# Kernel tuning notes

Measured on AMD Instinct MI355X. Metric: run time of the kernel, lower is better.

The kernel has to match this reference:

```python
import jax, jax.numpy as jnp
import numpy as np

E, H, F, K = 8, 1024, 4096, 2  # experts, hidden, intermediate, top-k
B, S = 4, 2048


def setup_inputs() -> dict:
    key = jax.random.key(0)
    ks = jax.random.split(key, 6)
    x = jax.random.normal(ks[0], (B, S, H), dtype=jnp.float32)
    gate_w = jax.random.normal(ks[1], (H, E), dtype=jnp.float32) * 0.02
    gate_b = jnp.zeros((E,), dtype=jnp.float32)
    Wg = jax.random.normal(ks[2], (E, H, F), dtype=jnp.float32) * 0.02
    Wu = jax.random.normal(ks[3], (E, H, F), dtype=jnp.float32) * 0.02
    Wd = jax.random.normal(ks[4], (E, F, H), dtype=jnp.float32) * 0.02
    return {"x": x, "gate_w": gate_w, "gate_b": gate_b, "Wg": Wg, "Wu": Wu, "Wd": Wd}


def _moe_forward(x, gate_w, gate_b, Wg, Wu, Wd):
    xf = x.reshape(-1, x.shape[-1])                      # [T, H]
    T = xf.shape[0]
    logits = xf @ gate_w + gate_b                        # [T, E]  (gate_logit)
    top_vals, top_idx = jax.lax.top_k(logits, K)         # [T, K]
    # scatter top-k logits into -inf background, softmax -> zero weight for unselected experts
    sparse = jnp.full_like(logits, -jnp.inf)
    sparse = sparse.at[jnp.arange(T)[:, None], top_idx].set(top_vals)
    gate_weights = jax.nn.softmax(sparse, axis=-1)       # [T, E], exactly 0 off top-k

    # sum_e w_e * Expert_e(x); scan over the small expert axis to bound memory
    def expert_step(acc, params):
        wg, wu, wd, w = params                           # wg:[H,F] wu:[H,F] wd:[F,H] w:[T]
        h = jax.nn.silu(xf @ wg) * (xf @ wu)             # [T, F]
        y = h @ wd                                       # [T, H]
        return acc + w[:, None] * y, None

    acc0 = jnp.zeros_like(xf)
    acc, _ = jax.lax.scan(expert_step, acc0, (Wg, Wu, Wd, gate_weights.T))
    return acc.reshape(x.shape), logits


def reference(x, gate_w, gate_b, Wg, Wu, Wd):
    return _moe_forward(x, gate_w, gate_b, Wg, Wu, Wd)
```

## Files before the change

### kernel.cpp

```cpp
#include <hip/hip_runtime.h>
#include <cstdint>

#define TTOK 8192
#define HID  1024
#define FFD  4096
#define NEXP 8
#define NASSIGN 16384

typedef __attribute__((ext_vector_type(8))) short bf16x8;
typedef __attribute__((ext_vector_type(4))) float f32x4;

__device__ __forceinline__ unsigned short f2bf(float f) {
  unsigned int u = __builtin_bit_cast(unsigned int, f);
  u += 0x7FFFu + ((u >> 16) & 1u);
  return (unsigned short)(u >> 16);
}

__device__ __forceinline__ void gload16(const unsigned short* g, unsigned short* l) {
  __builtin_amdgcn_global_load_lds(
      (const __attribute__((address_space(1))) unsigned int*)g,
      (__attribute__((address_space(3))) unsigned int*)l, 16, 0, 0);
}

__device__ __forceinline__ int swz_col(int t) {
  return (((t & 3) ^ ((t >> 3) & 3)) << 3);
}


__global__ void zero_counts_kernel(int* counts) {
  if (threadIdx.x < NEXP) counts[threadIdx.x] = 0;
}

__global__ void gate_kernel(const float* __restrict__ x,
                            const float* __restrict__ gw,
                            const float* __restrict__ gb,
                            float* __restrict__ logits_out,
                            int* __restrict__ counts,
                            int* __restrict__ te, int* __restrict__ tp,
                            float* __restrict__ tw) {
  const int lane = threadIdx.x & 63;
  const int wib  = threadIdx.x >> 6;
  const int t = blockIdx.x * 4 + wib;
  const float* xr = x + (size_t)t * HID;

  float acc[NEXP];
#pragma unroll
  for (int e = 0; e < NEXP; ++e) acc[e] = 0.f;

#pragma unroll
  for (int i = 0; i < HID / 64; ++i) {
    int h = lane + 64 * i;
    float xv = xr[h];
    const float* g = gw + h * NEXP;
#pragma unroll
    for (int e = 0; e < NEXP; ++e) acc[e] += xv * g[e];
  }
#pragma unroll
  for (int off = 32; off; off >>= 1)
#pragma unroll
    for (int e = 0; e < NEXP; ++e) acc[e] += __shfl_xor(acc[e], off);
#pragma unroll
  for (int e = 0; e < NEXP; ++e) acc[e] += gb[e];

  if (lane < NEXP) logits_out[(size_t)t * NEXP + lane] = acc[lane];

  if (lane == 0) {
    int e0 = 0; float v0 = acc[0];
#pragma unroll
    for (int e = 1; e < NEXP; ++e) if (acc[e] > v0) { v0 = acc[e]; e0 = e; }
    int e1 = -1; float v1 = -3.4e38f;
#pragma unroll
    for (int e = 0; e < NEXP; ++e) if (e != e0 && acc[e] > v1) { v1 = acc[e]; e1 = e; }
    float s = __expf(v1 - v0);
    float w0 = 1.f / (1.f + s);
    float w1 = s * w0;
    int p0 = atomicAdd(&counts[e0], 1);
    int p1 = atomicAdd(&counts[e1], 1);
    te[t * 2] = e0; te[t * 2 + 1] = e1;
    tp[t * 2] = p0; tp[t * 2 + 1] = p1;
    tw[t * 2] = w0; tw[t * 2 + 1] = w1;
  }
}

__global__ void scatter_kernel(const int* __restrict__ counts, int* __restrict__ offsets,
                               const int* __restrict__ te, const int* __restrict__ tp,
                               const float* __restrict__ tw,
                               int* __restrict__ tok_of, float* __restrict__ wt_of,
                               int* __restrict__ asn_of) {
  __shared__ int offs[NEXP];
  if (threadIdx.x == 0) {
    int run = 0;
    for (int e = 0; e < NEXP; ++e) { offs[e] = run; offsets[e] = run; run += counts[e]; }
  }
  __syncthreads();
  for (int t = threadIdx.x; t < TTOK; t += blockDim.x) {
#pragma unroll
    for (int j = 0; j < 2; ++j) {
      int e = te[t * 2 + j];
      int a = offs[e] + tp[t * 2 + j];
      tok_of[a] = t;
      wt_of[a] = tw[t * 2 + j];
      asn_of[t * 2 + j] = a;
    }
  }
}


__global__ void convert_x_kernel(const float* __restrict__ x, unsigned short* __restrict__ xb) {
  size_t i = ((size_t)blockIdx.x * 256 + threadIdx.x) * 8;
  float4 a = *(const float4*)(x + i);
  float4 b = *(const float4*)(x + i + 4);
  union { unsigned short us[8]; uint4 v; } u;
  u.us[0] = f2bf(a.x); u.us[1] = f2bf(a.y); u.us[2] = f2bf(a.z); u.us[3] = f2bf(a.w);
  u.us[4] = f2bf(b.x); u.us[5] = f2bf(b.y); u.us[6] = f2bf(b.z); u.us[7] = f2bf(b.w);
  *(uint4*)(xb + i) = u.v;
}

__global__ void transpose_cvt_kernel(const float* __restrict__ src,
                                     unsigned short* __restrict__ dst, int R, int C) {
  __shared__ float tile[32][33];
  const int r0 = blockIdx.y * 32, c0 = blockIdx.x * 32;
  const size_t base = (size_t)blockIdx.z * R * C;
  src += base; dst += base;
#pragma unroll
  for (int i = threadIdx.y; i < 32; i += 8)
    tile[i][threadIdx.x] = src[(size_t)(r0 + i) * C + c0 + threadIdx.x];
  __syncthreads();
#pragma unroll
  for (int i = threadIdx.y; i < 32; i += 8)
    dst[(size_t)(c0 + i) * R + r0 + threadIdx.x] = f2bf(tile[threadIdx.x][i]);
}


#define UBM 256
#define UBN 128
#define BK  32

__global__ __launch_bounds__(512, 2) void moe_up_kernel(
    const unsigned short* __restrict__ xb,
    const unsigned short* __restrict__ WgT,
    const unsigned short* __restrict__ WuT,
    const int* __restrict__ counts, const int* __restrict__ offsets,
    const int* __restrict__ tok_of,
    unsigned short* __restrict__ hbuf)
{
  const int e = blockIdx.x & 7;
  const int mblk = blockIdx.x >> 3;
  const int cnt = counts[e];
  if (mblk * UBM >= cnt) return;
  const int off = offsets[e];
  const int n0 = blockIdx.y * UBN;

  __shared__ __align__(16) unsigned short As[4 * UBM * BK];
  __shared__ __align__(16) unsigned short Bgs[4 * UBN * BK];
  __shared__ __align__(16) unsigned short Bus[4 * UBN * BK];
  __shared__ int toks[UBM];

  const int tid = threadIdx.x;
  const int lane = tid & 63;
  const int w = tid >> 6;

  for (int i = tid; i < UBM; i += 512) {
    int a = off + mblk * UBM + i;
    if (a > NASSIGN - 1) a = NASSIGN - 1;
    toks[i] = tok_of[a];
  }
  __syncthreads();

  const int trow = tid >> 2;
  const int tcol = swz_col(tid);
  const unsigned short* a_src0 = xb + (size_t)toks[trow] * HID + tcol;
  const unsigned short* a_src1 = xb + (size_t)toks[128 + trow] * HID + tcol;
  const unsigned short* bg_src = WgT + ((size_t)e * FFD + n0 + trow) * HID + tcol;
  const unsigned short* bu_src = WuT + ((size_t)e * FFD + n0 + trow) * HID + tcol;

  auto STAGE_A = [&](int kt) {
    const int b = kt & 3, k0 = kt * BK;
    gload16(a_src0 + k0, As + b * (UBM * BK) + tid * 8);
    gload16(a_src1 + k0, As + b * (UBM * BK) + 4096 + tid * 8);
  };
  auto STAGE_B = [&](int kt) {
    const int b = kt & 3, k0 = kt * BK;
    gload16(bg_src + k0, Bgs + b * (UBN * BK) + tid * 8);
    gload16(bu_src + k0, Bus + b * (UBN * BK) + tid * 8);
  };

  const int lr = lane & 15, s = lane >> 4;
  const int rdswz = ((s ^ ((lr >> 1) & 3)) << 3);
  const int wm = w >> 1, wn = w & 1;
  const int arow = wm * 64 + lr;
  const int brow = wn * 64 + lr;

  f32x4 accg[4][4] = {};
  f32x4 accu[4][4] = {};

  STAGE_A(0); STAGE_B(0);
  STAGE_A(1); STAGE_B(1);
  STAGE_A(2); STAGE_B(2);

  const int NT = HID / BK;
#pragma unroll 4
  for (int kt = 0; kt < NT; ++kt) {
    const int b = kt & 3;
    asm volatile("s_waitcnt vmcnt(8)" ::: "memory");
    __builtin_amdgcn_s_barrier();

    const unsigned short* ab = As  + b * (UBM * BK);
    const unsigned short* gb = Bgs + b * (UBN * BK);
    const unsigned short* ub = Bus + b * (UBN * BK);

    bf16x8 af[4], bgf[4];
#pragma unroll
    for (int m = 0; m < 4; ++m)
      af[m] = *(const bf16x8*)(ab + (arow + m * 16) * BK + rdswz);
#pragma unroll
    for (int n = 0; n < 4; ++n)
      bgf[n] = *(const bf16x8*)(gb + (brow + n * 16) * BK + rdswz);
    if (kt + 3 < NT) STAGE_A(kt + 3);
    __builtin_amdgcn_s_barrier();

    __builtin_amdgcn_s_setprio(1);
#pragma unroll
    for (int m = 0; m < 4; ++m)
#pragma unroll
      for (int n = 0; n < 4; ++n)
        accg[m][n] = __builtin_amdgcn_mfma_f32_16x16x32_bf16(af[m], bgf[n], accg[m][n], 0, 0, 0);
    __builtin_amdgcn_s_setprio(0);

    bf16x8 buf_[4];
#pragma unroll
    for (int n = 0; n < 4; ++n)
      buf_[n] = *(const bf16x8*)(ub + (brow + n * 16) * BK + rdswz);
    if (kt + 3 < NT) STAGE_B(kt + 3);
    __builtin_amdgcn_s_barrier();

    __builtin_amdgcn_s_setprio(1);
#pragma unroll
    for (int m = 0; m < 4; ++m)
#pragma unroll
      for (int n = 0; n < 4; ++n)
        accu[m][n] = __builtin_amdgcn_mfma_f32_16x16x32_bf16(af[m], buf_[n], accu[m][n], 0, 0, 0);
    __builtin_amdgcn_s_setprio(0);
  }

  const int crb = (lane >> 4) * 4, cc = lane & 15;
#pragma unroll
  for (int m = 0; m < 4; ++m)
#pragma unroll
    for (int n = 0; n < 4; ++n)
#pragma unroll
      for (int r = 0; r < 4; ++r) {
        int lrow = wm * 64 + m * 16 + crb + r;
        int grow = mblk * UBM + lrow;
        if (grow < cnt) {
          size_t a = (size_t)off + grow;
          float g = accg[m][n][r];
          float u = accu[m][n][r];
          float sg = g / (1.0f + __expf(-g));
          hbuf[a * FFD + (n0 + wn * 64 + n * 16 + cc)] = f2bf(sg * u);
        }
      }
}

#define DBM 128
#define DBN 256

__global__ __launch_bounds__(512, 2) void moe_down_kernel(
    const unsigned short* __restrict__ hb,
    const unsigned short* __restrict__ WdT,
    const int* __restrict__ counts, const int* __restrict__ offsets,
    float* __restrict__ ypart)
{
  const int e = blockIdx.x & 7;
  const int mblk = blockIdx.x >> 3;
  const int cnt = counts[e];
  if (mblk * DBM >= cnt) return;
  const int off = offsets[e];
  const int n0 = blockIdx.y * DBN;

  __shared__ __align__(16) unsigned short As[4 * DBM * BK];
  __shared__ __align__(16) unsigned short Bs[4 * DBN * BK];

  const int tid = threadIdx.x;
  const int lane = tid & 63;
  const int w = tid >> 6;

  const int trow = tid >> 2;
  const int tcol = swz_col(tid);
  int arow_g = off + mblk * DBM + trow;
  if (arow_g > NASSIGN - 1) arow_g = NASSIGN - 1;
  const unsigned short* a_src  = hb + (size_t)arow_g * FFD + tcol;
  const unsigned short* b_src0 = WdT + ((size_t)e * HID + n0 + trow) * FFD + tcol;
  const unsigned short* b_src1 = WdT + ((size_t)e * HID + n0 + 128 + trow) * FFD + tcol;

  auto STAGE = [&](int kt) {
    const int b = kt & 3, k0 = kt * BK;
    gload16(a_src  + k0, As + b * (DBM * BK) + tid * 8);
    gload16(b_src0 + k0, Bs + b * (DBN * BK) + tid * 8);
    gload16(b_src1 + k0, Bs + b * (DBN * BK) + 4096 + tid * 8);
  };

  const int lr = lane & 15, s = lane >> 4;
  const int rdswz = ((s ^ ((lr >> 1) & 3)) << 3);
  const int wm = w >> 2, wn = w & 3;
  const int arow = wm * 64 + lr;
  const int brow = wn * 64 + lr;

  f32x4 acc[4][4] = {};

  STAGE(0); STAGE(1); STAGE(2);

  const int NT = FFD / BK;
#pragma unroll 4
  for (int kt = 0; kt < NT; ++kt) {
    const int b = kt & 3;
    asm volatile("s_waitcnt vmcnt(6)" ::: "memory");
    __builtin_amdgcn_s_barrier();

    const unsigned short* ab = As + b * (DBM * BK);
    const unsigned short* bb = Bs + b * (DBN * BK);

    bf16x8 af[4], bf_[4];
#pragma unroll
    for (int m = 0; m < 4; ++m)
      af[m] = *(const bf16x8*)(ab + (arow + m * 16) * BK + rdswz);
#pragma unroll
    for (int n = 0; n < 4; ++n)
      bf_[n] = *(const bf16x8*)(bb + (brow + n * 16) * BK + rdswz);
    if (kt + 3 < NT) STAGE(kt + 3);
    __builtin_amdgcn_s_barrier();

    __builtin_amdgcn_s_setprio(1);
#pragma unroll
    for (int m = 0; m < 4; ++m)
#pragma unroll
      for (int n = 0; n < 4; ++n)
        acc[m][n] = __builtin_amdgcn_mfma_f32_16x16x32_bf16(af[m], bf_[n], acc[m][n], 0, 0, 0);
    __builtin_amdgcn_s_setprio(0);
  }

  const int crb = (lane >> 4) * 4, cc = lane & 15;
#pragma unroll
  for (int m = 0; m < 4; ++m)
#pragma unroll
    for (int n = 0; n < 4; ++n)
#pragma unroll
      for (int r = 0; r < 4; ++r) {
        int lrow = wm * 64 + m * 16 + crb + r;
        int grow = mblk * DBM + lrow;
        if (grow < cnt)
          ypart[((size_t)off + grow) * HID + (n0 + wn * 64 + n * 16 + cc)] = acc[m][n][r];
      }
}

__global__ void combine_kernel(const float* __restrict__ ypart,
                               const int* __restrict__ asn_of,
                               const float* __restrict__ wt_of,
                               float* __restrict__ y) {
  const int t = blockIdx.x;
  const int a0 = asn_of[t * 2], a1 = asn_of[t * 2 + 1];
  const float w0 = wt_of[a0], w1 = wt_of[a1];
  const int c = threadIdx.x * 4;
  float4 p0 = *(const float4*)&ypart[(size_t)a0 * HID + c];
  float4 p1 = *(const float4*)&ypart[(size_t)a1 * HID + c];
  float4 r;
  r.x = w0 * p0.x + w1 * p1.x;
  r.y = w0 * p0.y + w1 * p1.y;
  r.z = w0 * p0.z + w1 * p1.z;
  r.w = w0 * p0.w + w1 * p1.w;
  *(float4*)&y[(size_t)t * HID + c] = r;
}


extern "C" void kernel_launch(void* const* d_in, const int* in_sizes, int n_in,
                              void* d_out, int out_size, void* d_ws, size_t ws_size,
                              hipStream_t stream) {
  const float* x  = (const float*)d_in[0];
  const float* gw = (const float*)d_in[1];
  const float* gb = (const float*)d_in[2];
  const float* Wg = (const float*)d_in[3];
  const float* Wu = (const float*)d_in[4];
  const float* Wd = (const float*)d_in[5];
  float* out = (float*)d_out;
  float* logits = out + (size_t)TTOK * HID;

  char* ws = (char*)d_ws;
  size_t o = 0;
  auto carve = [&](size_t b) { char* p = ws + o; o += (b + 255) & ~(size_t)255; return p; };
  int*   counts  = (int*)carve(NEXP * 4);
  int*   offsets = (int*)carve(NEXP * 4);
  int*   te      = (int*)carve((size_t)TTOK * 2 * 4);
  int*   tp      = (int*)carve((size_t)TTOK * 2 * 4);
  float* tw      = (float*)carve((size_t)TTOK * 2 * 4);
  int*   tok_of  = (int*)carve((size_t)NASSIGN * 4);
  float* wt_of   = (float*)carve((size_t)NASSIGN * 4);
  int*   asn_of  = (int*)carve((size_t)TTOK * 2 * 4);
  unsigned short* xb  = (unsigned short*)carve((size_t)TTOK * HID * 2);
  unsigned short* WgT = (unsigned short*)carve((size_t)NEXP * FFD * HID * 2);
  unsigned short* WuT = (unsigned short*)carve((size_t)NEXP * FFD * HID * 2);
  unsigned short* WdT = (unsigned short*)carve((size_t)NEXP * HID * FFD * 2);
  unsigned short* hb  = (unsigned short*)carve((size_t)NASSIGN * FFD * 2);
  float* ypart        = (float*)carve((size_t)NASSIGN * HID * 4);
  (void)ws_size; (void)in_sizes; (void)n_in; (void)out_size;

  zero_counts_kernel<<<dim3(1), dim3(64), 0, stream>>>(counts);
  gate_kernel<<<dim3(TTOK / 4), dim3(256), 0, stream>>>(x, gw, gb, logits, counts, te, tp, tw);
  scatter_kernel<<<dim3(1), dim3(256), 0, stream>>>(counts, offsets, te, tp, tw, tok_of, wt_of, asn_of);
  convert_x_kernel<<<dim3((TTOK * HID) / 2048), dim3(256), 0, stream>>>(x, xb);
  transpose_cvt_kernel<<<dim3(FFD / 32, HID / 32, NEXP), dim3(32, 8), 0, stream>>>(Wg, WgT, HID, FFD);
  transpose_cvt_kernel<<<dim3(FFD / 32, HID / 32, NEXP), dim3(32, 8), 0, stream>>>(Wu, WuT, HID, FFD);
  transpose_cvt_kernel<<<dim3(HID / 32, FFD / 32, NEXP), dim3(32, 8), 0, stream>>>(Wd, WdT, FFD, HID);
  moe_up_kernel<<<dim3(NEXP * 32, FFD / UBN), dim3(512), 0, stream>>>(xb, WgT, WuT, counts, offsets, tok_of, hb);
  moe_down_kernel<<<dim3(NEXP * 64, HID / DBN), dim3(512), 0, stream>>>(hb, WdT, counts, offsets, ypart);
  combine_kernel<<<dim3(TTOK), dim3(256), 0, stream>>>(ypart, asn_of, wt_of, out);
}
```

Measured before the change: 1.084 ms.

## Rework MoE GEMM pipelines to BK=64 double-buffered tiles with larger down-proj tile

```diff
diff --git a/kernel.cpp b/kernel.cpp
--- a/kernel.cpp
+++ b/kernel.cpp
@@ -20,10 +20,6 @@
   __builtin_amdgcn_global_load_lds(
       (const __attribute__((address_space(1))) unsigned int*)g,
       (__attribute__((address_space(3))) unsigned int*)l, 16, 0, 0);
-}
-
-__device__ __forceinline__ int swz_col(int t) {
-  return (((t & 3) ^ ((t >> 3) & 3)) << 3);
 }
 
 
@@ -132,11 +128,12 @@
 }
 
 
+#define BK 64
+
 #define UBM 256
 #define UBN 128
-#define BK  32
-
-__global__ __launch_bounds__(512, 2) void moe_up_kernel(
+
+__global__ __launch_bounds__(512, 1) void moe_up_kernel(
     const unsigned short* __restrict__ xb,
     const unsigned short* __restrict__ WgT,
     const unsigned short* __restrict__ WuT,
@@ -151,9 +148,9 @@
   const int off = offsets[e];
   const int n0 = blockIdx.y * UBN;
 
-  __shared__ __align__(16) unsigned short As[4 * UBM * BK];
-  __shared__ __align__(16) unsigned short Bgs[4 * UBN * BK];
-  __shared__ __align__(16) unsigned short Bus[4 * UBN * BK];
+  __shared__ __align__(16) unsigned short As[2][UBM * BK];
+  __shared__ __align__(16) unsigned short Bgs[2][UBN * BK];
+  __shared__ __align__(16) unsigned short Bus[2][UBN * BK];
   __shared__ int toks[UBM];
 
   const int tid = threadIdx.x;
@@ -167,105 +164,124 @@
   }
   __syncthreads();
 
-  const int trow = tid >> 2;
-  const int tcol = swz_col(tid);
-  const unsigned short* a_src0 = xb + (size_t)toks[trow] * HID + tcol;
-  const unsigned short* a_src1 = xb + (size_t)toks[128 + trow] * HID + tcol;
-  const unsigned short* bg_src = WgT + ((size_t)e * FFD + n0 + trow) * HID + tcol;
-  const unsigned short* bu_src = WuT + ((size_t)e * FFD + n0 + trow) * HID + tcol;
-
-  auto STAGE_A = [&](int kt) {
-    const int b = kt & 3, k0 = kt * BK;
-    gload16(a_src0 + k0, As + b * (UBM * BK) + tid * 8);
-    gload16(a_src1 + k0, As + b * (UBM * BK) + 4096 + tid * 8);
+  const int st = tid & 7, sr = tid >> 3;
+  const int scol = ((st ^ (sr & 7)) << 3);
+  const unsigned short* a_src[4];
+#pragma unroll
+  for (int i = 0; i < 4; ++i)
+    a_src[i] = xb + (size_t)toks[i * 64 + sr] * HID + scol;
+  const unsigned short* bg_src[2];
+  const unsigned short* bu_src[2];
+#pragma unroll
+  for (int i = 0; i < 2; ++i) {
+    bg_src[i] = WgT + ((size_t)e * FFD + n0 + i * 64 + sr) * HID + scol;
+    bu_src[i] = WuT + ((size_t)e * FFD + n0 + i * 64 + sr) * HID + scol;
+  }
+
+  auto STAGE = [&](int kt) {
+    const int b = kt & 1, k0 = kt * BK;
+#pragma unroll
+    for (int i = 0; i < 4; ++i) gload16(a_src[i] + k0, &As[b][i * 4096 + tid * 8]);
+#pragma unroll
+    for (int i = 0; i < 2; ++i) {
+      gload16(bg_src[i] + k0, &Bgs[b][i * 4096 + tid * 8]);
+      gload16(bu_src[i] + k0, &Bus[b][i * 4096 + tid * 8]);
+    }
   };
-  auto STAGE_B = [&](int kt) {
-    const int b = kt & 3, k0 = kt * BK;
-    gload16(bg_src + k0, Bgs + b * (UBN * BK) + tid * 8);
-    gload16(bu_src + k0, Bus + b * (UBN * BK) + tid * 8);
-  };
-
-  const int lr = lane & 15, s = lane >> 4;
-  const int rdswz = ((s ^ ((lr >> 1) & 3)) << 3);
-  const int wm = w >> 1, wn = w & 1;
-  const int arow = wm * 64 + lr;
-  const int brow = wn * 64 + lr;
-
-  f32x4 accg[4][4] = {};
-  f32x4 accu[4][4] = {};
-
-  STAGE_A(0); STAGE_B(0);
-  STAGE_A(1); STAGE_B(1);
-  STAGE_A(2); STAGE_B(2);
+
+  const int lr = lane & 15, lq = lane >> 4;
+  const int sA0 = (((0 * 4 + lq) ^ (lr & 7)) << 3);
+  const int sA1 = (((1 * 4 + lq) ^ (lr & 7)) << 3);
+  const int wm = w >> 2, wn = w & 3;
+
+  f32x4 accg[8][2] = {};
+  f32x4 accu[8][2] = {};
+
+  STAGE(0);
 
   const int NT = HID / BK;
-#pragma unroll 4
+#pragma unroll 1
   for (int kt = 0; kt < NT; ++kt) {
-    const int b = kt & 3;
-    asm volatile("s_waitcnt vmcnt(8)" ::: "memory");
+    const int b = kt & 1;
+    if (kt + 1 < NT) {
+      STAGE(kt + 1);
+      asm volatile("s_waitcnt vmcnt(8)" ::: "memory");
+    } else {
+      asm volatile("s_waitcnt vmcnt(0)" ::: "memory");
+    }
     __builtin_amdgcn_s_barrier();
 
-    const unsigned short* ab = As  + b * (UBM * BK);
-    const unsigned short* gb = Bgs + b * (UBN * BK);
-    const unsigned short* ub = Bus + b * (UBN * BK);
-
-    bf16x8 af[4], bgf[4];
-#pragma unroll
-    for (int m = 0; m < 4; ++m)
-      af[m] = *(const bf16x8*)(ab + (arow + m * 16) * BK + rdswz);
-#pragma unroll
-    for (int n = 0; n < 4; ++n)
-      bgf[n] = *(const bf16x8*)(gb + (brow + n * 16) * BK + rdswz);
-    if (kt + 3 < NT) STAGE_A(kt + 3);
-    __builtin_amdgcn_s_barrier();
-
-    __builtin_amdgcn_s_setprio(1);
-#pragma unroll
-    for (int m = 0; m < 4; ++m)
-#pragma unroll
-      for (int n = 0; n < 4; ++n)
-        accg[m][n] = __builtin_amdgcn_mfma_f32_16x16x32_bf16(af[m], bgf[n], accg[m][n], 0, 0, 0);
-    __builtin_amdgcn_s_setprio(0);
-
-    bf16x8 buf_[4];
-#pragma unroll
-    for (int n = 0; n < 4; ++n)
-      buf_[n] = *(const bf16x8*)(ub + (brow + n * 16) * BK + rdswz);
-    if (kt + 3 < NT) STAGE_B(kt + 3);
-    __builtin_amdgcn_s_barrier();
-
-    __builtin_amdgcn_s_setprio(1);
-#pragma unroll
-    for (int m = 0; m < 4; ++m)
-#pragma unroll
-      for (int n = 0; n < 4; ++n)
-        accu[m][n] = __builtin_amdgcn_mfma_f32_16x16x32_bf16(af[m], buf_[n], accu[m][n], 0, 0, 0);
-    __builtin_amdgcn_s_setprio(0);
+    const unsigned short* Ab = As[b];
+    const unsigned short* Gb = Bgs[b];
+    const unsigned short* Ub = Bus[b];
+    bf16x8 af[4], bg[2], bu[2];
+
+#pragma unroll
+    for (int ks = 0; ks < 2; ++ks) {
+      const int sA = ks ? sA1 : sA0;
+#pragma unroll
+      for (int m = 0; m < 4; ++m)
+        af[m] = *(const bf16x8*)(Ab + (wm * 128 + m * 16 + lr) * BK + sA);
+#pragma unroll
+      for (int nn = 0; nn < 2; ++nn) {
+        bg[nn] = *(const bf16x8*)(Gb + (wn * 32 + nn * 16 + lr) * BK + sA);
+        bu[nn] = *(const bf16x8*)(Ub + (wn * 32 + nn * 16 + lr) * BK + sA);
+      }
+      __builtin_amdgcn_s_barrier();
+      asm volatile("s_waitcnt lgkmcnt(0)" ::: "memory");
+      __builtin_amdgcn_sched_barrier(0);
+      __builtin_amdgcn_s_setprio(1);
+#pragma unroll
+      for (int m = 0; m < 4; ++m)
+#pragma unroll
+        for (int nn = 0; nn < 2; ++nn) {
+          accg[m][nn] = __builtin_amdgcn_mfma_f32_16x16x32_bf16(af[m], bg[nn], accg[m][nn], 0, 0, 0);
+          accu[m][nn] = __builtin_amdgcn_mfma_f32_16x16x32_bf16(af[m], bu[nn], accu[m][nn], 0, 0, 0);
+        }
+      __builtin_amdgcn_s_setprio(0);
+      __builtin_amdgcn_s_barrier();
+#pragma unroll
+      for (int m = 0; m < 4; ++m)
+        af[m] = *(const bf16x8*)(Ab + (wm * 128 + 64 + m * 16 + lr) * BK + sA);
+      __builtin_amdgcn_s_barrier();
+      asm volatile("s_waitcnt lgkmcnt(0)" ::: "memory");
+      __builtin_amdgcn_sched_barrier(0);
+      __builtin_amdgcn_s_setprio(1);
+#pragma unroll
+      for (int m = 0; m < 4; ++m)
+#pragma unroll
+        for (int nn = 0; nn < 2; ++nn) {
+          accg[4 + m][nn] = __builtin_amdgcn_mfma_f32_16x16x32_bf16(af[m], bg[nn], accg[4 + m][nn], 0, 0, 0);
+          accu[4 + m][nn] = __builtin_amdgcn_mfma_f32_16x16x32_bf16(af[m], bu[nn], accu[4 + m][nn], 0, 0, 0);
+        }
+      __builtin_amdgcn_s_setprio(0);
+      __builtin_amdgcn_s_barrier();
+    }
   }
 
   const int crb = (lane >> 4) * 4, cc = lane & 15;
 #pragma unroll
-  for (int m = 0; m < 4; ++m)
-#pragma unroll
-    for (int n = 0; n < 4; ++n)
+  for (int m = 0; m < 8; ++m)
+#pragma unroll
+    for (int nn = 0; nn < 2; ++nn)
 #pragma unroll
       for (int r = 0; r < 4; ++r) {
-        int lrow = wm * 64 + m * 16 + crb + r;
+        int lrow = wm * 128 + m * 16 + crb + r;
         int grow = mblk * UBM + lrow;
         if (grow < cnt) {
           size_t a = (size_t)off + grow;
-          float g = accg[m][n][r];
-          float u = accu[m][n][r];
+          float g = accg[m][nn][r];
+          float u = accu[m][nn][r];
           float sg = g / (1.0f + __expf(-g));
-          hbuf[a * FFD + (n0 + wn * 64 + n * 16 + cc)] = f2bf(sg * u);
+          hbuf[a * FFD + (n0 + wn * 32 + nn * 16 + cc)] = f2bf(sg * u);
         }
       }
 }
 
-#define DBM 128
+#define DBM 256
 #define DBN 256
 
-__global__ __launch_bounds__(512, 2) void moe_down_kernel(
+__global__ __launch_bounds__(512, 1) void moe_down_kernel(
     const unsigned short* __restrict__ hb,
     const unsigned short* __restrict__ WdT,
     const int* __restrict__ counts, const int* __restrict__ offsets,
@@ -278,75 +294,104 @@
   const int off = offsets[e];
   const int n0 = blockIdx.y * DBN;
 
-  __shared__ __align__(16) unsigned short As[4 * DBM * BK];
-  __shared__ __align__(16) unsigned short Bs[4 * DBN * BK];
+  __shared__ __align__(16) unsigned short As[2][DBM * BK];
+  __shared__ __align__(16) unsigned short Bs[2][DBN * BK];
 
   const int tid = threadIdx.x;
   const int lane = tid & 63;
   const int w = tid >> 6;
 
-  const int trow = tid >> 2;
-  const int tcol = swz_col(tid);
-  int arow_g = off + mblk * DBM + trow;
-  if (arow_g > NASSIGN - 1) arow_g = NASSIGN - 1;
-  const unsigned short* a_src  = hb + (size_t)arow_g * FFD + tcol;
-  const unsigned short* b_src0 = WdT + ((size_t)e * HID + n0 + trow) * FFD + tcol;
-  const unsigned short* b_src1 = WdT + ((size_t)e * HID + n0 + 128 + trow) * FFD + tcol;
+  const int st = tid & 7, sr = tid >> 3;
+  const int scol = ((st ^ (sr & 7)) << 3);
+  const unsigned short* a_src[4];
+  const unsigned short* b_src[4];
+#pragma unroll
+  for (int i = 0; i < 4; ++i) {
+    int ar = off + mblk * DBM + i * 64 + sr;
+    if (ar > NASSIGN - 1) ar = NASSIGN - 1;
+    a_src[i] = hb + (size_t)ar * FFD + scol;
+    b_src[i] = WdT + ((size_t)e * HID + n0 + i * 64 + sr) * FFD + scol;
+  }
 
   auto STAGE = [&](int kt) {
-    const int b = kt & 3, k0 = kt * BK;
-    gload16(a_src  + k0, As + b * (DBM * BK) + tid * 8);
-    gload16(b_src0 + k0, Bs + b * (DBN * BK) + tid * 8);
-    gload16(b_src1 + k0, Bs + b * (DBN * BK) + 4096 + tid * 8);
+    const int b = kt & 1, k0 = kt * BK;
+#pragma unroll
+    for (int i = 0; i < 4; ++i) {
+      gload16(a_src[i] + k0, &As[b][i * 4096 + tid * 8]);
+      gload16(b_src[i] + k0, &Bs[b][i * 4096 + tid * 8]);
+    }
   };
 
-  const int lr = lane & 15, s = lane >> 4;
-  const int rdswz = ((s ^ ((lr >> 1) & 3)) << 3);
+  const int lr = lane & 15, lq = lane >> 4;
+  const int sA0 = (((0 * 4 + lq) ^ (lr & 7)) << 3);
+  const int sA1 = (((1 * 4 + lq) ^ (lr & 7)) << 3);
   const int wm = w >> 2, wn = w & 3;
-  const int arow = wm * 64 + lr;
-  const int brow = wn * 64 + lr;
-
-  f32x4 acc[4][4] = {};
-
-  STAGE(0); STAGE(1); STAGE(2);
+
+  f32x4 acc[8][4] = {};
+
+  STAGE(0);
 
   const int NT = FFD / BK;
-#pragma unroll 4
+#pragma unroll 1
   for (int kt = 0; kt < NT; ++kt) {
-    const int b = kt & 3;
-    asm volatile("s_waitcnt vmcnt(6)" ::: "memory");
+    const int b = kt & 1;
+    if (kt + 1 < NT) {
+      STAGE(kt + 1);
+      asm volatile("s_waitcnt vmcnt(8)" ::: "memory");
+    } else {
+      asm volatile("s_waitcnt vmcnt(0)" ::: "memory");
+    }
     __builtin_amdgcn_s_barrier();
 
-    const unsigned short* ab = As + b * (DBM * BK);
-    const unsigned short* bb = Bs + b * (DBN * BK);
-
+    const unsigned short* Ab = As[b];
+    const unsigned short* Bb = Bs[b];
     bf16x8 af[4], bf_[4];
-#pragma unroll
-    for (int m = 0; m < 4; ++m)
-      af[m] = *(const bf16x8*)(ab + (arow + m * 16) * BK + rdswz);
+
+#pragma unroll
+    for (int ks = 0; ks < 2; ++ks) {
+      const int sA = ks ? sA1 : sA0;
+#pragma unroll
+      for (int m = 0; m < 4; ++m)
+        af[m] = *(const bf16x8*)(Ab + (wm * 128 + m * 16 + lr) * BK + sA);
+#pragma unroll
+      for (int n = 0; n < 4; ++n)
+        bf_[n] = *(const bf16x8*)(Bb + (wn * 64 + n * 16 + lr) * BK + sA);
+      __builtin_amdgcn_s_barrier();
+      asm volatile("s_waitcnt lgkmcnt(0)" ::: "memory");
+      __builtin_amdgcn_sched_barrier(0);
+      __builtin_amdgcn_s_setprio(1);
+#pragma unroll
+      for (int m = 0; m < 4; ++m)
+#pragma unroll
+        for (int n = 0; n < 4; ++n)
+          acc[m][n] = __builtin_amdgcn_mfma_f32_16x16x32_bf16(af[m], bf_[n], acc[m][n], 0, 0, 0);
+      __builtin_amdgcn_s_setprio(0);
+      __builtin_amdgcn_s_barrier();
+#pragma unroll
+      for (int m = 0; m < 4; ++m)
+        af[m] = *(const bf16x8*)(Ab + (wm * 128 + 64 + m * 16 + lr) * BK + sA);
+      __builtin_amdgcn_s_barrier();
+      asm volatile("s_waitcnt lgkmcnt(0)" ::: "memory");
+      __builtin_amdgcn_sched_barrier(0);
+      __builtin_amdgcn_s_setprio(1);
+#pragma unroll
+      for (int m = 0; m < 4; ++m)
+#pragma unroll
+        for (int n = 0; n < 4; ++n)
+          acc[4 + m][n] = __builtin_amdgcn_mfma_f32_16x16x32_bf16(af[m], bf_[n], acc[4 + m][n], 0, 0, 0);
+      __builtin_amdgcn_s_setprio(0);
+      __builtin_amdgcn_s_barrier();
+    }
+  }
+
+  const int crb = (lane >> 4) * 4, cc = lane & 15;
+#pragma unroll
+  for (int m = 0; m < 8; ++m)
 #pragma unroll
     for (int n = 0; n < 4; ++n)
-      bf_[n] = *(const bf16x8*)(bb + (brow + n * 16) * BK + rdswz);
-    if (kt + 3 < NT) STAGE(kt + 3);
-    __builtin_amdgcn_s_barrier();
-
-    __builtin_amdgcn_s_setprio(1);
-#pragma unroll
-    for (int m = 0; m < 4; ++m)
-#pragma unroll
-      for (int n = 0; n < 4; ++n)
-        acc[m][n] = __builtin_amdgcn_mfma_f32_16x16x32_bf16(af[m], bf_[n], acc[m][n], 0, 0, 0);
-    __builtin_amdgcn_s_setprio(0);
-  }
-
-  const int crb = (lane >> 4) * 4, cc = lane & 15;
-#pragma unroll
-  for (int m = 0; m < 4; ++m)
-#pragma unroll
-    for (int n = 0; n < 4; ++n)
 #pragma unroll
       for (int r = 0; r < 4; ++r) {
-        int lrow = wm * 64 + m * 16 + crb + r;
+        int lrow = wm * 128 + m * 16 + crb + r;
         int grow = mblk * DBM + lrow;
         if (grow < cnt)
           ypart[((size_t)off + grow) * HID + (n0 + wn * 64 + n * 16 + cc)] = acc[m][n][r];
@@ -411,6 +456,6 @@
   transpose_cvt_kernel<<<dim3(FFD / 32, HID / 32, NEXP), dim3(32, 8), 0, stream>>>(Wu, WuT, HID, FFD);
   transpose_cvt_kernel<<<dim3(HID / 32, FFD / 32, NEXP), dim3(32, 8), 0, stream>>>(Wd, WdT, FFD, HID);
   moe_up_kernel<<<dim3(NEXP * 32, FFD / UBN), dim3(512), 0, stream>>>(xb, WgT, WuT, counts, offsets, tok_of, hb);
-  moe_down_kernel<<<dim3(NEXP * 64, HID / DBN), dim3(512), 0, stream>>>(hb, WdT, counts, offsets, ypart);
+  moe_down_kernel<<<dim3(NEXP * 32, HID / DBN), dim3(512), 0, stream>>>(hb, WdT, counts, offsets, ypart);
   combine_kernel<<<dim3(TTOK), dim3(256), 0, stream>>>(ypart, asn_of, wt_of, out);
 }
```

New measurement: 1.307 ms. 20.5% more time.
